# Kernel tuning notes

Measured on AMD Instinct MI355X. Metric: run time of the kernel, lower is better.

The kernel has to match this reference:

```python
import jax, jax.numpy as jnp
import numpy as np

N_NODES = 50000
N_EDGES = 312500
IN_F = 256
OUT_F = 256


def setup_inputs() -> dict:
    key = jax.random.key(0)
    kx, ki, kj, kw, kb = jax.random.split(key, 5)
    x = jax.random.normal(kx, (N_NODES, IN_F), dtype=jnp.float32)
    Ai = jax.random.randint(ki, (N_EDGES,), 0, N_NODES, dtype=jnp.int64)
    Aj = jax.random.randint(kj, (N_EDGES,), 0, N_NODES, dtype=jnp.int64)
    # Linear(2*in_features, out_features): PyTorch default uniform(-1/sqrt(fan_in), 1/sqrt(fan_in))
    bound = 1.0 / np.sqrt(2 * IN_F)
    W = jax.random.uniform(kw, (OUT_F, 2 * IN_F), dtype=jnp.float32, minval=-bound, maxval=bound)
    b = jax.random.uniform(kb, (OUT_F,), dtype=jnp.float32, minval=-bound, maxval=bound)
    return {"x": x, "W": W, "b": b, "Ai": Ai, "Aj": Aj}


def reference(x, W, b, Ai, Aj):
    X_i = x[Ai]                      # [E, F] gather source rows
    X_j = x[Aj]                      # [E, F]
    X_ij = jnp.concatenate([X_i, X_j], axis=1)   # [E, 2F]
    E_msg = jnp.einsum('ef,of->eo', X_ij, W) + b  # [E, out]
    agg_xi = jax.ops.segment_sum(E_msg, Ai, num_segments=N_NODES)  # [N, out]
    return agg_xi
```

## Files before the change

### kernel.cpp

```cpp
#include <hip/hip_runtime.h>
#include <hip/hip_bf16.h>

#define NN 50000
#define NE 312500
#define FIN 256
#define NT 1564
#define CAP 64

typedef __attribute__((ext_vector_type(4))) float f32x4;
typedef __attribute__((ext_vector_type(2))) float f32x2;
typedef __attribute__((ext_vector_type(8))) short bf16x8;
typedef __attribute__((ext_vector_type(4))) unsigned short u16x4;
typedef __attribute__((ext_vector_type(8))) unsigned short u16x8;
typedef __attribute__((ext_vector_type(4))) unsigned int u32x4;

#ifndef __has_builtin
#define __has_builtin(x) 0
#endif
#if __has_builtin(__builtin_amdgcn_cvt_pk_f32_fp8) && __has_builtin(__builtin_amdgcn_cvt_pk_fp8_f32)
#define HWFP8 1
#else
#define HWFP8 0
#endif

__device__ __forceinline__ float bf2f(unsigned short u) {
  return __builtin_bit_cast(float, ((unsigned int)u) << 16);
}
__device__ __forceinline__ unsigned short f2bf(float f) {
  return __builtin_bit_cast(unsigned short, __float2bfloat16(f));
}

#if !HWFP8
__device__ __forceinline__ unsigned enc8(float f) {
  unsigned bits = __builtin_bit_cast(unsigned, f);
  unsigned s = bits >> 31;
  unsigned a = bits & 0x7FFFFFFFu;
  if (a < 0x3C400000u) return s << 7;
  a += 0x0007FFFFu + ((a >> 20) & 1);
  unsigned e = (a >> 23) - 120u;
  unsigned m = (a >> 20) & 7u;
  if (e > 15u) { e = 15u; m = 6u; }
  return (s << 7) | (e << 3) | m;
}
__device__ __forceinline__ float dec8(unsigned b) {
  unsigned s = (b >> 7) & 1u, e = (b >> 3) & 15u, m = b & 7u;
  float v = e ? __builtin_bit_cast(float, ((e + 120u) << 23) | (m << 20))
              : (float)m * 0.001953125f;
  return s ? -v : v;
}
#endif

__device__ __forceinline__ unsigned enc4fp8(float a, float b, float c, float d) {
#if HWFP8
  int pk = __builtin_amdgcn_cvt_pk_fp8_f32(a, b, 0, false);
  pk = __builtin_amdgcn_cvt_pk_fp8_f32(c, d, pk, true);
  return (unsigned)pk;
#else
  return enc8(a) | (enc8(b) << 8) | (enc8(c) << 16) | (enc8(d) << 24);
#endif
}

__device__ __forceinline__ void dec4fp8(unsigned w, float* r) {
#if HWFP8
  f32x2 lo = __builtin_amdgcn_cvt_pk_f32_fp8((int)w, false);
  f32x2 hi = __builtin_amdgcn_cvt_pk_f32_fp8((int)w, true);
  r[0] = lo[0]; r[1] = lo[1]; r[2] = hi[0]; r[3] = hi[1];
#else
  r[0] = dec8(w & 255); r[1] = dec8((w >> 8) & 255);
  r[2] = dec8((w >> 16) & 255); r[3] = dec8(w >> 24);
#endif
}

__device__ __forceinline__ bf16x8 cvt8v(f32x4 a, f32x4 b) {
  bf16x8 r;
  #pragma unroll
  for (int i = 0; i < 4; ++i) {
    r[i]     = (short)f2bf(a[i]);
    r[i + 4] = (short)f2bf(b[i]);
  }
  return r;
}

__device__ __forceinline__ bf16x8 cvt8(const float* p) {
  return cvt8v(*(const f32x4*)p, *(const f32x4*)(p + 4));
}

__global__ __launch_bounds__(256) void k_wz(const float* __restrict__ W,
                                            unsigned short* __restrict__ WbP,
                                            int* __restrict__ deg) {
  if (blockIdx.x >= 64) {
    int i = (blockIdx.x - 64) * 256 + threadIdx.x;
    if (i < 50048) deg[i] = 0;
    return;
  }
  int lane = threadIdx.x & 63, wid = threadIdx.x >> 6;
  int c = blockIdx.x * 4 + wid;
  int o16 = c >> 3, kk = c & 7;
  int lr = lane & 15, lk = lane >> 4;
  int o = o16 * 16 + lr;
  int k = kk * 32 + lk * 8;
  const float* src = (o < 256) ? (W + (size_t)o * 512 + k)
                               : (W + (size_t)(o - 256) * 512 + 256 + k);
  *(bf16x8*)(WbP + (size_t)c * 512 + lane * 8) = cvt8(src);
}

__global__ __launch_bounds__(512) void k_gemm(
    const float* __restrict__ x, const unsigned short* __restrict__ WbP,
    unsigned short* __restrict__ Y1b, unsigned char* __restrict__ Y2f8,
    const int* __restrict__ Ai, const int* __restrict__ Aj,
    int* __restrict__ deg, int* __restrict__ edst) {
  __shared__ __align__(16) unsigned short A[2][8192];
  const int tid = threadIdx.x;
  const int lane = tid & 63, w = tid >> 6;
  const int lr = lane & 15, lk = lane >> 4;

  for (int e = blockIdx.x * 512 + tid; e < NE; e += 256 * 512) {
    int a = Ai[e];
    int p = atomicAdd(&deg[a], 1);
    edst[a * CAP + p] = Aj[e];
  }

  bf16x8 B[8][4];
  #pragma unroll
  for (int kk = 0; kk < 8; ++kk)
    #pragma unroll
    for (int n = 0; n < 4; ++n)
      B[kk][n] = *(const bf16x8*)(WbP + ((size_t)(w * 4 + n) * 8 + kk) * 512 + lane * 8);
  #pragma unroll
  for (int kk = 0; kk < 8; ++kk)
    #pragma unroll
    for (int n = 0; n < 4; ++n)
      asm volatile("" : "+v"(B[kk][n]));

  const int row0 = (tid >> 5);
  const int seg = tid & 31;
  const int uoff0 = ((row0 >> 4) * 8 + (seg >> 2)) * 512 +
                    (((((seg & 3) * 16) + (row0 & 15)) * 8) ^ ((seg & 7) << 3));
  const int row1 = 16 + row0;
  const int uoff1 = ((row1 >> 4) * 8 + (seg >> 2)) * 512 +
                    (((((seg & 3) * 16) + (row1 & 15)) * 8) ^ ((seg & 7) << 3));

  int tile = blockIdx.x;
  {
    int g0 = tile * 32 + row0; if (g0 > NN - 1) g0 = NN - 1;
    int g1 = tile * 32 + row1; if (g1 > NN - 1) g1 = NN - 1;
    const float* s0 = x + (size_t)g0 * FIN + seg * 8;
    const float* s1 = x + (size_t)g1 * FIN + seg * 8;
    f32x4 a0 = *(const f32x4*)s0, b0 = *(const f32x4*)(s0 + 4);
    f32x4 a1 = *(const f32x4*)s1, b1 = *(const f32x4*)(s1 + 4);
    *(bf16x8*)(&A[0][uoff0]) = cvt8v(a0, b0);
    *(bf16x8*)(&A[0][uoff1]) = cvt8v(a1, b1);
  }
  __syncthreads();

  int p = 0;
  for (; tile < NT; tile += 256) {
    const int nxt = tile + 256;
    const bool hn = (nxt < NT);

    f32x4 a0, b0, a1, b1;
    if (hn) {
      int g0 = nxt * 32 + row0; if (g0 > NN - 1) g0 = NN - 1;
      int g1 = nxt * 32 + row1; if (g1 > NN - 1) g1 = NN - 1;
      const float* s0 = x + (size_t)g0 * FIN + seg * 8;
      const float* s1 = x + (size_t)g1 * FIN + seg * 8;
      a0 = *(const f32x4*)s0; b0 = *(const f32x4*)(s0 + 4);
      a1 = *(const f32x4*)s1; b1 = *(const f32x4*)(s1 + 4);
    }

    f32x4 acc[2][4];
    #pragma unroll
    for (int rg = 0; rg < 2; ++rg)
      #pragma unroll
      for (int n = 0; n < 4; ++n) acc[rg][n] = (f32x4){0.f, 0.f, 0.f, 0.f};
    #pragma unroll
    for (int rg = 0; rg < 2; ++rg) {
      #pragma unroll
      for (int kk = 0; kk < 8; ++kk) {
        bf16x8 af = *(const bf16x8*)(
            &A[p][(rg * 8 + kk) * 512 + ((lane * 8) ^ (((kk & 1) << 5) | (lk << 3)))]);
        #pragma unroll
        for (int n = 0; n < 4; ++n)
          acc[rg][n] = __builtin_amdgcn_mfma_f32_16x16x32_bf16(af, B[kk][n], acc[rg][n], 0, 0, 0);
      }
    }

    #pragma unroll
    for (int rg = 0; rg < 2; ++rg) {
      #pragma unroll
      for (int rr = 0; rr < 4; ++rr) {
        int row = tile * 32 + rg * 16 + lk * 4 + rr;
        if (w < 4) {
          u16x4 v;
          #pragma unroll
          for (int n = 0; n < 4; ++n)
            v[n] = f2bf(acc[rg][n][rr]);
          *(u16x4*)(Y1b + (size_t)row * 256 + w * 64 + lr * 4) = v;
        } else {
          unsigned pk = enc4fp8(acc[rg][0][rr], acc[rg][1][rr],
                                acc[rg][2][rr], acc[rg][3][rr]);
          *(unsigned int*)(Y2f8 + (size_t)row * 256 + (w - 4) * 64 + lr * 4) = pk;
        }
      }
    }

    if (hn) {
      *(bf16x8*)(&A[p ^ 1][uoff0]) = cvt8v(a0, b0);
      *(bf16x8*)(&A[p ^ 1][uoff1]) = cvt8v(a1, b1);
      __syncthreads();
    }
    p ^= 1;
  }
}

__global__ __launch_bounds__(256) void k_epi(
    const unsigned short* __restrict__ Y1b, const unsigned char* __restrict__ Y2f8,
    const int* __restrict__ deg, const int* __restrict__ edst,
    const float* __restrict__ bias, float* __restrict__ out) {
  __shared__ float sm[1024];
  int wid = threadIdx.x >> 6;
  int lane = threadIdx.x & 63;
  int es = lane >> 4;
  int fg = lane & 15;
  int n = blockIdx.x * 4 + wid;
  if (n >= NN) return;
  int o = n * CAP;
  int c = deg[n];

  u16x8 y10 = *(const u16x8*)(Y1b + (size_t)n * 256 + fg * 16);
  u16x8 y11 = *(const u16x8*)(Y1b + (size_t)n * 256 + fg * 16 + 8);

  const unsigned char* Y2 = Y2f8 + fg * 16;
  f32x4 ac[4];
  #pragma unroll
  for (int h = 0; h < 4; ++h) ac[h] = (f32x4){0.f, 0.f, 0.f, 0.f};

  int e = es;
  for (; e + 4 < c; e += 8) {
    int jA = edst[o + e];
    int jB = edst[o + e + 4];
    u32x4 vA = *(const u32x4*)(Y2 + (size_t)jA * 256);
    u32x4 vB = *(const u32x4*)(Y2 + (size_t)jB * 256);
    #pragma unroll
    for (int h = 0; h < 4; ++h) {
      float rA[4], rB[4];
      dec4fp8(vA[h], rA);
      dec4fp8(vB[h], rB);
      #pragma unroll
      for (int i = 0; i < 4; ++i) ac[h][i] += rA[i] + rB[i];
    }
  }
  if (e < c) {
    int j = edst[o + e];
    u32x4 v = *(const u32x4*)(Y2 + (size_t)j * 256);
    #pragma unroll
    for (int h = 0; h < 4; ++h) {
      float r[4];
      dec4fp8(v[h], r);
      #pragma unroll
      for (int i = 0; i < 4; ++i) ac[h][i] += r[i];
    }
  }

  #pragma unroll
  for (int h = 0; h < 4; ++h)
    #pragma unroll
    for (int i = 0; i < 4; ++i) {
      ac[h][i] += __shfl_xor(ac[h][i], 16);
      ac[h][i] += __shfl_xor(ac[h][i], 32);
    }

  float* Wm = sm + wid * 256;
  if (es == 0) {
    float dg = (float)c;
    #pragma unroll
    for (int i = 0; i < 16; ++i) {
      int p = fg * 16 + i;
      int tc = (p & ~63) | ((p & 3) << 4) | ((p >> 2) & 15);
      float y1 = bf2f((i < 8) ? y10[i] : y11[i - 8]);
      Wm[tc] = dg * (y1 + bias[tc]) + ac[i >> 2][i & 3];
    }
  }
  asm volatile("s_waitcnt lgkmcnt(0)" ::: "memory");
  f32x4 res = *(const f32x4*)(Wm + lane * 4);
  __builtin_nontemporal_store(res, (f32x4*)out + (size_t)n * 64 + lane);
}

extern "C" void kernel_launch(void* const* d_in, const int* in_sizes, int n_in,
                              void* d_out, int out_size, void* d_ws, size_t ws_size,
                              hipStream_t stream) {
  const float* x = (const float*)d_in[0];
  const float* W = (const float*)d_in[1];
  const float* b = (const float*)d_in[2];
  const int* Ai = (const int*)d_in[3];
  const int* Aj = (const int*)d_in[4];
  float* out = (float*)d_out;

  int* ip = (int*)d_ws;
  int* deg  = ip;
  int* edst = ip + 50048;
  unsigned short* WbP  = (unsigned short*)(ip + 3253120);
  unsigned short* Y1b  = (unsigned short*)(ip + 3318656);
  unsigned char*  Y2f8 = (unsigned char*)(ip + 9724800);

  k_wz<<<260, 256, 0, stream>>>(W, WbP, deg);
  k_gemm<<<256, 512, 0, stream>>>(x, WbP, Y1b, Y2f8, Ai, Aj, deg, edst);
  k_epi<<<12500, 256, 0, stream>>>(Y1b, Y2f8, deg, edst, b, out);
}
```

Measured before the change: 71.91 us.

## Stage weights in LDS per output half and load activations directly to registers

The GEMM kernel is restructured so each block handles one output half (the Y1 or the Y2 family) and stages that half's bf16 weights (128 KB) into LDS with global_load_lds. Activations are no longer double-buffered through LDS. Each wave now loads its x rows straight into registers, converts them to bf16, and computes a 32x128 tile, reading B fragments from LDS. This removes the per-tile __syncthreads and the LDS round-trip for A, and lets a wave do more MFMAs per A fragment. The cost is more LDS reads of B per tile, a 128 KB LDS footprint that may limit occupancy despite the launch bound of 2, and exposed global-load latency without explicit prefetch.

```diff
diff --git a/kernel.cpp b/kernel.cpp
--- a/kernel.cpp
+++ b/kernel.cpp
@@ -3,7 +3,6 @@
 
 #define NN 50000
 #define NE 312500
-#define FIN 256
 #define NT 1564
 #define CAP 64
 
@@ -104,15 +103,17 @@
   *(bf16x8*)(WbP + (size_t)c * 512 + lane * 8) = cvt8(src);
 }
 
-__global__ __launch_bounds__(512) void k_gemm(
+__global__ __launch_bounds__(512, 2) void k_gemm(
     const float* __restrict__ x, const unsigned short* __restrict__ WbP,
     unsigned short* __restrict__ Y1b, unsigned char* __restrict__ Y2f8,
     const int* __restrict__ Ai, const int* __restrict__ Aj,
     int* __restrict__ deg, int* __restrict__ edst) {
-  __shared__ __align__(16) unsigned short A[2][8192];
+  __shared__ __align__(16) unsigned short Blds[65536];
   const int tid = threadIdx.x;
   const int lane = tid & 63, w = tid >> 6;
   const int lr = lane & 15, lk = lane >> 4;
+  const int fam = blockIdx.x >> 7;
+  const int bid = blockIdx.x & 127;
 
   for (int e = blockIdx.x * 512 + tid; e < NE; e += 256 * 512) {
     int a = Ai[e];
@@ -120,96 +121,85 @@
     edst[a * CAP + p] = Aj[e];
   }
 
-  bf16x8 B[8][4];
-  #pragma unroll
-  for (int kk = 0; kk < 8; ++kk)
-    #pragma unroll
-    for (int n = 0; n < 4; ++n)
-      B[kk][n] = *(const bf16x8*)(WbP + ((size_t)(w * 4 + n) * 8 + kk) * 512 + lane * 8);
-  #pragma unroll
-  for (int kk = 0; kk < 8; ++kk)
-    #pragma unroll
-    for (int n = 0; n < 4; ++n)
-      asm volatile("" : "+v"(B[kk][n]));
-
-  const int row0 = (tid >> 5);
-  const int seg = tid & 31;
-  const int uoff0 = ((row0 >> 4) * 8 + (seg >> 2)) * 512 +
-                    (((((seg & 3) * 16) + (row0 & 15)) * 8) ^ ((seg & 7) << 3));
-  const int row1 = 16 + row0;
-  const int uoff1 = ((row1 >> 4) * 8 + (seg >> 2)) * 512 +
-                    (((((seg & 3) * 16) + (row1 & 15)) * 8) ^ ((seg & 7) << 3));
-
-  int tile = blockIdx.x;
-  {
-    int g0 = tile * 32 + row0; if (g0 > NN - 1) g0 = NN - 1;
-    int g1 = tile * 32 + row1; if (g1 > NN - 1) g1 = NN - 1;
-    const float* s0 = x + (size_t)g0 * FIN + seg * 8;
-    const float* s1 = x + (size_t)g1 * FIN + seg * 8;
-    f32x4 a0 = *(const f32x4*)s0, b0 = *(const f32x4*)(s0 + 4);
-    f32x4 a1 = *(const f32x4*)s1, b1 = *(const f32x4*)(s1 + 4);
-    *(bf16x8*)(&A[0][uoff0]) = cvt8v(a0, b0);
-    *(bf16x8*)(&A[0][uoff1]) = cvt8v(a1, b1);
+  #pragma unroll
+  for (int i = 0; i < 16; ++i) {
+    int ch = w * 16 + i;
+    __builtin_amdgcn_global_load_lds(
+        (const __attribute__((address_space(1))) void*)(
+            WbP + ((size_t)(fam * 128 + ch)) * 512 + lane * 8),
+        (__attribute__((address_space(3))) void*)(Blds + ch * 512 + lane * 8),
+        16, 0, 0);
   }
   __syncthreads();
 
-  int p = 0;
-  for (; tile < NT; tile += 256) {
-    const int nxt = tile + 256;
-    const bool hn = (nxt < NT);
-
-    f32x4 a0, b0, a1, b1;
-    if (hn) {
-      int g0 = nxt * 32 + row0; if (g0 > NN - 1) g0 = NN - 1;
-      int g1 = nxt * 32 + row1; if (g1 > NN - 1) g1 = NN - 1;
-      const float* s0 = x + (size_t)g0 * FIN + seg * 8;
-      const float* s1 = x + (size_t)g1 * FIN + seg * 8;
-      a0 = *(const f32x4*)s0; b0 = *(const f32x4*)(s0 + 4);
-      a1 = *(const f32x4*)s1; b1 = *(const f32x4*)(s1 + 4);
-    }
-
-    f32x4 acc[2][4];
+  const int g = w & 1;
+  const int rslot = w >> 1;
+
+  for (int t = bid * 4 + rslot; t < NT; t += 512) {
+    const int rbase = t * 32;
+
+    f32x4 P[16][2];
+    #pragma unroll
+    for (int rg = 0; rg < 2; ++rg) {
+      int row = rbase + rg * 16 + lr;
+      if (row > NN - 1) row = NN - 1;
+      const float* xp = x + (size_t)row * 256 + lk * 8;
+      #pragma unroll
+      for (int kk = 0; kk < 8; ++kk) {
+        P[rg * 8 + kk][0] = *(const f32x4*)(xp + kk * 32);
+        P[rg * 8 + kk][1] = *(const f32x4*)(xp + kk * 32 + 4);
+      }
+    }
+    bf16x8 A[2][8];
     #pragma unroll
     for (int rg = 0; rg < 2; ++rg)
       #pragma unroll
-      for (int n = 0; n < 4; ++n) acc[rg][n] = (f32x4){0.f, 0.f, 0.f, 0.f};
+      for (int kk = 0; kk < 8; ++kk)
+        A[rg][kk] = cvt8v(P[rg * 8 + kk][0], P[rg * 8 + kk][1]);
+
+    f32x4 acc[2][8];
+    #pragma unroll
+    for (int rg = 0; rg < 2; ++rg)
+      #pragma unroll
+      for (int c = 0; c < 8; ++c) acc[rg][c] = (f32x4){0.f, 0.f, 0.f, 0.f};
+
+    #pragma unroll
+    for (int kk = 0; kk < 8; ++kk) {
+      bf16x8 Bf[8];
+      #pragma unroll
+      for (int c = 0; c < 8; ++c)
+        Bf[c] = *(const bf16x8*)(Blds + ((g * 8 + c) * 8 + kk) * 512 + lane * 8);
+      #pragma unroll
+      for (int rg = 0; rg < 2; ++rg)
+        #pragma unroll
+        for (int c = 0; c < 8; ++c)
+          acc[rg][c] = __builtin_amdgcn_mfma_f32_16x16x32_bf16(A[rg][kk], Bf[c], acc[rg][c], 0, 0, 0);
+    }
+
     #pragma unroll
     for (int rg = 0; rg < 2; ++rg) {
       #pragma unroll
-      for (int kk = 0; kk < 8; ++kk) {
-        bf16x8 af = *(const bf16x8*)(
-            &A[p][(rg * 8 + kk) * 512 + ((lane * 8) ^ (((kk & 1) << 5) | (lk << 3)))]);
-        #pragma unroll
-        for (int n = 0; n < 4; ++n)
-          acc[rg][n] = __builtin_amdgcn_mfma_f32_16x16x32_bf16(af, B[kk][n], acc[rg][n], 0, 0, 0);
-      }
-    }
-
-    #pragma unroll
-    for (int rg = 0; rg < 2; ++rg) {
-      #pragma unroll
       for (int rr = 0; rr < 4; ++rr) {
-        int row = tile * 32 + rg * 16 + lk * 4 + rr;
-        if (w < 4) {
-          u16x4 v;
+        int row = rbase + rg * 16 + lk * 4 + rr;
+        if (fam == 0) {
           #pragma unroll
-          for (int n = 0; n < 4; ++n)
-            v[n] = f2bf(acc[rg][n][rr]);
-          *(u16x4*)(Y1b + (size_t)row * 256 + w * 64 + lr * 4) = v;
+          for (int st = 0; st < 2; ++st) {
+            u16x4 v;
+            #pragma unroll
+            for (int n = 0; n < 4; ++n)
+              v[n] = f2bf(acc[rg][st * 4 + n][rr]);
+            *(u16x4*)(Y1b + (size_t)row * 256 + g * 128 + st * 64 + lr * 4) = v;
+          }
         } else {
-          unsigned pk = enc4fp8(acc[rg][0][rr], acc[rg][1][rr],
-                                acc[rg][2][rr], acc[rg][3][rr]);
-          *(unsigned int*)(Y2f8 + (size_t)row * 256 + (w - 4) * 64 + lr * 4) = pk;
+          #pragma unroll
+          for (int st = 0; st < 2; ++st) {
+            unsigned pk = enc4fp8(acc[rg][st * 4 + 0][rr], acc[rg][st * 4 + 1][rr],
+                                  acc[rg][st * 4 + 2][rr], acc[rg][st * 4 + 3][rr]);
+            *(unsigned int*)(Y2f8 + (size_t)row * 256 + g * 128 + st * 64 + lr * 4) = pk;
+          }
         }
       }
     }
-
-    if (hn) {
-      *(bf16x8*)(&A[p ^ 1][uoff0]) = cvt8v(a0, b0);
-      *(bf16x8*)(&A[p ^ 1][uoff1]) = cvt8v(a1, b1);
-      __syncthreads();
-    }
-    p ^= 1;
   }
 }
 
```

New measurement: 126.4 us. +75.8%, slower.
